# Optimization experiments

Hardware: AMD Instinct MI355X
Metric: run time of the kernel (lower is better)

The kernel has to match this reference:

```python
import jax, jax.numpy as jnp
import numpy as np

B, SEQ, D, N_LAYERS, HEADS, D_FF = 256, 43, 18, 6, 3, 2048
A_MAX, NB = 128, 7
EPS = 1e-6


def _norm(x, a, b):
    mu = x.mean(-1, keepdims=True)
    sd = jnp.std(x, axis=-1, ddof=1, keepdims=True)  # torch std is unbiased
    return a * (x - mu) / (sd + EPS) + b


def _attn(x, Wq, bq, Wk, bk, Wv, bv, Wo, bo, mask):
    b_, s, d = x.shape
    dk = d // HEADS
    def split_heads(W, bb):
        return (x @ W + bb).reshape(b_, s, HEADS, dk).transpose(0, 2, 1, 3)
    q, k, v = split_heads(Wq, bq), split_heads(Wk, bk), split_heads(Wv, bv)
    scores = jnp.einsum('bhqd,bhkd->bhqk', q, k) / jnp.sqrt(jnp.float32(dk))
    scores = jnp.where(mask[:, None, :, :] == 0, -1e9, scores)  # mask [B,1,S] -> [B,1,1,S]
    attn = jax.nn.softmax(scores, axis=-1)
    o = jnp.einsum('bhqk,bhkd->bhqd', attn, v).transpose(0, 2, 1, 3).reshape(b_, s, d)
    return o @ Wo + bo


def setup_inputs() -> dict:
    key = jax.random.key(0)
    ks = iter(jax.random.split(key, 40))
    g = lambda shape, s=0.05: jax.random.normal(next(ks), shape, dtype=jnp.float32) * s
    inp = {
        'src': jax.random.normal(next(ks), (B, SEQ, D), dtype=jnp.float32),
        'mask': jnp.ones((B, 1, SEQ), dtype=jnp.int32),
        'max_atoms': A_MAX,
        'enc_Wq': g((N_LAYERS, D, D)), 'enc_bq': g((N_LAYERS, D)),
        'enc_Wk': g((N_LAYERS, D, D)), 'enc_bk': g((N_LAYERS, D)),
        'enc_Wv': g((N_LAYERS, D, D)), 'enc_bv': g((N_LAYERS, D)),
        'enc_Wo': g((N_LAYERS, D, D)), 'enc_bo': g((N_LAYERS, D)),
        'enc_ln1_a': jnp.ones((N_LAYERS, D), jnp.float32), 'enc_ln1_b': jnp.zeros((N_LAYERS, D), jnp.float32),
        'enc_ln2_a': jnp.ones((N_LAYERS, D), jnp.float32), 'enc_ln2_b': jnp.zeros((N_LAYERS, D), jnp.float32),
        'enc_ffW1': g((N_LAYERS, D, D_FF)), 'enc_ffb1': g((N_LAYERS, D_FF)),
        'enc_ffW2': g((N_LAYERS, D_FF, D)), 'enc_ffb2': g((N_LAYERS, D)),
        'll2_W': g((D, A_MAX)), 'll2_b': g((A_MAX,)),
        'll_W': g((SEQ, A_MAX)), 'll_b': g((A_MAX,)),
        'fl_W': g((2 * A_MAX, NB)), 'fl_b': g((NB,)),
    }
    return inp


def reference(src, enc_Wq, enc_bq, enc_Wk, enc_bk, enc_Wv, enc_bv, enc_Wo, enc_bo,
              enc_ln1_a, enc_ln1_b, enc_ln2_a, enc_ln2_b,
              enc_ffW1, enc_ffb1, enc_ffW2, enc_ffb2,
              ll2_W, ll2_b, ll_W, ll_b, fl_W, fl_b, mask, max_atoms):
    # --- Encoder (dropout=0 at eval; no final norm, as in source) ---
    x = src
    for i in range(N_LAYERS):
        x2 = _norm(x, enc_ln1_a[i], enc_ln1_b[i])
        x = x + _attn(x2, enc_Wq[i], enc_bq[i], enc_Wk[i], enc_bk[i],
                      enc_Wv[i], enc_bv[i], enc_Wo[i], enc_bo[i], mask)
        x2 = _norm(x, enc_ln2_a[i], enc_ln2_b[i])
        x = x + (jax.nn.relu(x2 @ enc_ffW1[i] + enc_ffb1[i]) @ enc_ffW2[i] + enc_ffb2[i])
    # --- EdgeClassify2 ---
    red = x @ ll2_W + ll2_b            # [B, S, A]
    red = red.transpose(0, 2, 1)       # [B, A, S]
    R = red @ ll_W + ll_b              # [B, A, A]; repeat_e[:,i,i,:] == R[:,i,:]
    # final_e[b,i,j] = concat(R[b,i], R[b,j]); fl(concat) = R_i@W1 + R_j@W2 + b (exact)
    W1, W2 = fl_W[:max_atoms], fl_W[max_atoms:]
    P = R @ W1                          # [B, A, nb]
    Q = R @ W2                          # [B, A, nb]
    return P[:, :, None, :] + Q[:, None, :, :] + fl_b  # [B, A, A, nb]
```

## Files before the change

### kernel.cpp

```cpp
#include <hip/hip_runtime.h>
#include <math.h>

namespace {

constexpr int Sq = 43;
constexpr int Dm = 18;
constexpr int Dff = 2048;
constexpr int Am = 128;
constexpr int Nb = 7;
constexpr int NR = 11008;
constexpr int RSZ = NR * Dm;
constexpr float EPSf = 1e-6f;

typedef __attribute__((ext_vector_type(8))) short bf16x8;
typedef __attribute__((ext_vector_type(4))) float f32x4;

__device__ __forceinline__ bf16x8 FRAG(uint4 u) {
    return __builtin_bit_cast(bf16x8, u);
}
__device__ __forceinline__ unsigned BFPK(float a, float b) {
    return (__float_as_uint(a) >> 16) | (__float_as_uint(b) & 0xFFFF0000u);
}

__global__ __launch_bounds__(192) void k_attn(
    int layer,
    const float* __restrict__ Xi, float* __restrict__ Xn,
    float* __restrict__ x2g,
    const int* __restrict__ maskg,
    const float* __restrict__ Wq, const float* __restrict__ bq,
    const float* __restrict__ Wk, const float* __restrict__ bk,
    const float* __restrict__ Wv, const float* __restrict__ bv,
    const float* __restrict__ ln1a, const float* __restrict__ ln1b,
    const float* __restrict__ Wo, const float* __restrict__ bo,
    const float* __restrict__ ln2a, const float* __restrict__ ln2b,
    const float* __restrict__ b2g,
    const float* __restrict__ fW1g, const float* __restrict__ fW2g,
    uint4* __restrict__ W1F, uint4* __restrict__ W2F,
    const float* __restrict__ llW, const float* __restrict__ llb,
    const float* __restrict__ flW, const float* __restrict__ flb,
    const float* __restrict__ ll2b,
    float* __restrict__ Mw, float* __restrict__ PS1, float* __restrict__ QS2)
{
    __shared__ __align__(16) float ks[Sq * 20];
    __shared__ __align__(16) float vs[Sq * 20];
    __shared__ float os[Sq * Dm];
    __shared__ int ms[Sq];
    __shared__ float M[602];
    __shared__ float cc2[14];
    __shared__ float SS[14];

    const int tid = threadIdx.x;
    const int b = blockIdx.x;

    if (b >= 256) {
        if (b < 320) {
            for (int e = (b - 256) * 192 + tid; e < 98304; e += 12288) {
                const int lane = e & 63;
                const int s = (e >> 6) & 1;
                const int t = (e >> 7) & 1;
                const int c = (e >> 8) & 63;
                const int l = e >> 14;
                const int g = lane >> 4, m = lane & 15;
                {
                    const int j = c * 32 + t * 16 + m;
                    unsigned u[4] = {0u, 0u, 0u, 0u};
                    #pragma unroll
                    for (int i = 0; i < 8; i++) {
                        const int k = 8 * g + i;
                        float v = (k < 18)
                            ? fW1g[((size_t)l * Dm + k) * Dff + j] : 0.f;
                        unsigned hb = __float_as_uint(v) & 0xFFFF0000u;
                        unsigned bits;
                        if (s == 0) bits = hb >> 16;
                        else {
                            float lo = v - __uint_as_float(hb);
                            bits = (__float_as_uint(lo) & 0xFFFF0000u) >> 16;
                        }
                        u[i >> 1] |= bits << (16 * (i & 1));
                    }
                    W1F[e] = make_uint4(u[0], u[1], u[2], u[3]);
                }
                {
                    unsigned u[4] = {0u, 0u, 0u, 0u};
                    const int d = (t == 0) ? m : 16 + m;
                    const bool valid = (t == 0) || (m < 2);
                    #pragma unroll
                    for (int i = 0; i < 8; i++) {
                        const int j = c * 32 + 8 * g + i;
                        float v = valid
                            ? fW2g[((size_t)l * Dff + j) * Dm + d] : 0.f;
                        unsigned hb = __float_as_uint(v) & 0xFFFF0000u;
                        unsigned bits;
                        if (s == 0) bits = hb >> 16;
                        else {
                            float lo = v - __uint_as_float(hb);
                            bits = (__float_as_uint(lo) & 0xFFFF0000u) >> 16;
                        }
                        u[i >> 1] |= bits << (16 * (i & 1));
                    }
                    W2F[e] = make_uint4(u[0], u[1], u[2], u[3]);
                }
            }
            return;
        }
        for (int m = tid; m < 602; m += 192) {
            int half = m / 301, rem = m - half * 301;
            int s = rem / 7, n = rem - 7 * s;
            float a = 0.f;
            for (int jj = 0; jj < Am; jj++)
                a += llW[s * Am + jj] * flW[(half * Am + jj) * Nb + n];
            M[m] = a;
        }
        if (tid < 14) {
            int half = tid / 7, n = tid - 7 * (tid / 7);
            float a = 0.f;
            for (int jj = 0; jj < Am; jj++)
                a += llb[jj] * flW[(half * Am + jj) * Nb + n];
            cc2[tid] = a;
        }
        __syncthreads();
        if (tid < 14) {
            int half = tid / 7, n = tid - 7 * (tid / 7);
            float s2 = 0.f;
            for (int s = 0; s < Sq; s++) s2 += M[half * 301 + s * 7 + n];
            SS[tid] = s2;
        }
        __syncthreads();
        for (int m = tid; m < 602; m += 192) Mw[m] = M[m];
        for (int m = tid; m < 896; m += 192) {
            int i = m / 7, n = m - 7 * i;
            PS1[m] = cc2[n] + ll2b[i] * SS[n];
            QS2[m] = cc2[7 + n] + ll2b[i] * SS[7 + n] + flb[n];
        }
        return;
    }

    const float scale = 0.40824829046386296f;
    const int h = tid >> 6;
    const int q = tid & 63;

    if (tid < Sq) ms[tid] = maskg[b * Sq + tid];

    float y[Dm];
    float qv6[6];
    if (q < Sq) {
        const size_t ro = (size_t)(b * Sq + q) * Dm;
        #pragma unroll
        for (int k = 0; k < 9; k++) {
            float2 t = *(const float2*)(Xi + ro + 2 * k);
            y[2 * k] = t.x; y[2 * k + 1] = t.y;
        }
        float mu = 0.f;
        #pragma unroll
        for (int d = 0; d < Dm; d++) mu += y[d];
        mu *= (1.f / Dm);
        float var = 0.f;
        #pragma unroll
        for (int d = 0; d < Dm; d++) { float t = y[d] - mu; var += t * t; }
        var *= (1.f / (Dm - 1));
        float isd = 1.f / (sqrtf(var) + EPSf);
        float x2[Dm];
        #pragma unroll
        for (int d = 0; d < Dm; d++)
            x2[d] = ln1a[layer * Dm + d] * (y[d] - mu) * isd
                  + ln1b[layer * Dm + d];
        const float* wqp = Wq + layer * Dm * Dm;
        const float* wkp = Wk + layer * Dm * Dm;
        const float* wvp = Wv + layer * Dm * Dm;
        #pragma unroll
        for (int dh = 0; dh < 6; dh++) {
            const int d = h * 6 + dh;
            float aq = bq[layer * Dm + d];
            float ak = bk[layer * Dm + d];
            float av = bv[layer * Dm + d];
            #pragma unroll
            for (int dd = 0; dd < Dm; dd++) {
                aq += x2[dd] * wqp[dd * Dm + d];
                ak += x2[dd] * wkp[dd * Dm + d];
                av += x2[dd] * wvp[dd * Dm + d];
            }
            qv6[dh] = aq;
            ks[q * 20 + d] = ak;
            vs[q * 20 + d] = av;
        }
    }
    __syncthreads();

    if (q < Sq) {
        float sum = 0.f;
        float o6[6];
        #pragma unroll
        for (int d = 0; d < 6; d++) o6[d] = 0.f;
        const float q0 = qv6[0], q1 = qv6[1], q2 = qv6[2];
        const float q3 = qv6[3], q4 = qv6[4], q5 = qv6[5];
        for (int j = 0; j < Sq; j++) {
            const float* kr = ks + j * 20 + h * 6;
            const float2 k0 = *(const float2*)(kr);
            const float2 k1 = *(const float2*)(kr + 2);
            const float2 k2 = *(const float2*)(kr + 4);
            float t = q0 * k0.x + q1 * k0.y + q2 * k1.x +
                      q3 * k1.y + q4 * k2.x + q5 * k2.y;
            t *= scale;
            if (ms[j] == 0) t = -1e9f;
            float e = __expf(t);
            sum += e;
            const float* vr = vs + j * 20 + h * 6;
            const float2 v0 = *(const float2*)(vr);
            const float2 v1 = *(const float2*)(vr + 2);
            const float2 v2 = *(const float2*)(vr + 4);
            o6[0] += e * v0.x; o6[1] += e * v0.y; o6[2] += e * v1.x;
            o6[3] += e * v1.y; o6[4] += e * v2.x; o6[5] += e * v2.y;
        }
        float inv = 1.f / sum;
        #pragma unroll
        for (int d = 0; d < 6; d++) os[q * Dm + h * 6 + d] = o6[d] * inv;
    }
    __syncthreads();

    if (h == 0 && q < Sq) {
        const float* wo = Wo + layer * Dm * Dm;
        const float* orow = os + q * Dm;
        float yo[Dm];
        #pragma unroll 3
        for (int d = 0; d < Dm; d++) {
            float t = bo[layer * Dm + d];
            #pragma unroll
            for (int dd = 0; dd < Dm; dd++) t += orow[dd] * wo[dd * Dm + d];
            yo[d] = y[d] + t;
        }
        const size_t ro = (size_t)(b * Sq + q) * Dm;
        #pragma unroll
        for (int d = 0; d < Dm; d++)
            Xn[ro + d] = yo[d] + b2g[layer * Dm + d];
        float mu = 0.f;
        #pragma unroll
        for (int d = 0; d < Dm; d++) mu += yo[d];
        mu *= (1.f / Dm);
        float var = 0.f;
        #pragma unroll
        for (int d = 0; d < Dm; d++) { float t = yo[d] - mu; var += t * t; }
        var *= (1.f / (Dm - 1));
        float isd = 1.f / (sqrtf(var) + EPSf);
        #pragma unroll
        for (int d = 0; d < Dm; d++)
            x2g[ro + d] =
                ln2a[layer * Dm + d] * (yo[d] - mu) * isd + ln2b[layer * Dm + d];
    }
}

__global__ __launch_bounds__(256) void k_ffn(
    int layer, const float* __restrict__ x2g,
    const uint4* __restrict__ W1F, const uint4* __restrict__ W2F,
    const float* __restrict__ fb1g, float* __restrict__ Xn)
{
    __shared__ __align__(16) short Hbuf[4][2][640];

    const int tid  = threadIdx.x;
    const int lane = tid & 63;
    const int wv   = tid >> 6;
    const int g    = lane >> 4;
    const int m    = lane & 15;
    const int row  = blockIdx.x * 16 + m;

    unsigned bh[4] = {0u, 0u, 0u, 0u}, bl[4] = {0u, 0u, 0u, 0u};
    #pragma unroll
    for (int i = 0; i < 8; i++) {
        const int k = 8 * g + i;
        float v = (k < 18) ? x2g[(size_t)row * Dm + k] : 0.f;
        unsigned hbits = __float_as_uint(v) & 0xFFFF0000u;
        float lo = v - __uint_as_float(hbits);
        unsigned lbits = __float_as_uint(lo) & 0xFFFF0000u;
        bh[i >> 1] |= (hbits >> 16) << (16 * (i & 1));
        bl[i >> 1] |= (lbits >> 16) << (16 * (i & 1));
    }
    const bf16x8 Bxhi = FRAG(make_uint4(bh[0], bh[1], bh[2], bh[3]));
    const bf16x8 Bxlo = FRAG(make_uint4(bl[0], bl[1], bl[2], bl[3]));

    f32x4 y0 = {0.f, 0.f, 0.f, 0.f};
    f32x4 y1 = {0.f, 0.f, 0.f, 0.f};
    const uint4* w1b = W1F + (size_t)layer * 16384;
    const uint4* w2b = W2F + (size_t)layer * 16384;
    const float* b1b = fb1g + layer * Dff;
    short* Hh = &Hbuf[wv][0][0];
    short* Hl = &Hbuf[wv][1][0];

    const int c0 = wv * 16;
    for (int c = c0; c < c0 + 16; ++c) {
        #pragma unroll
        for (int t = 0; t < 2; ++t) {
            const uint4 ah = w1b[c * 256 + t * 128 + lane];
            const uint4 al = w1b[c * 256 + t * 128 + 64 + lane];
            f32x4 c1 = {0.f, 0.f, 0.f, 0.f};
            c1 = __builtin_amdgcn_mfma_f32_16x16x32_bf16(FRAG(ah), Bxhi, c1, 0, 0, 0);
            c1 = __builtin_amdgcn_mfma_f32_16x16x32_bf16(FRAG(al), Bxhi, c1, 0, 0, 0);
            c1 = __builtin_amdgcn_mfma_f32_16x16x32_bf16(FRAG(ah), Bxlo, c1, 0, 0, 0);
            const f32x4 bb = *(const f32x4*)(b1b + c * 32 + t * 16 + 4 * g);
            unsigned ph[2], pl[2];
            #pragma unroll
            for (int r2 = 0; r2 < 2; ++r2) {
                float h0 = fmaxf(c1[2 * r2] + bb[2 * r2], 0.f);
                float h1 = fmaxf(c1[2 * r2 + 1] + bb[2 * r2 + 1], 0.f);
                unsigned h0b = __float_as_uint(h0) & 0xFFFF0000u;
                unsigned h1b = __float_as_uint(h1) & 0xFFFF0000u;
                ph[r2] = (h0b >> 16) | h1b;
                float l0 = h0 - __uint_as_float(h0b);
                float l1 = h1 - __uint_as_float(h1b);
                pl[r2] = ((__float_as_uint(l0) & 0xFFFF0000u) >> 16)
                       | (__float_as_uint(l1) & 0xFFFF0000u);
            }
            const int joff = m * 40 + t * 16 + 4 * g;
            *(uint2*)&Hh[joff] = make_uint2(ph[0], ph[1]);
            *(uint2*)&Hl[joff] = make_uint2(pl[0], pl[1]);
        }
        const bf16x8 bH = FRAG(*(const uint4*)&Hh[m * 40 + 8 * g]);
        const bf16x8 bL = FRAG(*(const uint4*)&Hl[m * 40 + 8 * g]);
        const uint4 a0h = w2b[c * 256 + lane];
        const uint4 a0l = w2b[c * 256 + 64 + lane];
        const uint4 a1h = w2b[c * 256 + 128 + lane];
        const uint4 a1l = w2b[c * 256 + 192 + lane];
        y0 = __builtin_amdgcn_mfma_f32_16x16x32_bf16(FRAG(a0h), bH, y0, 0, 0, 0);
        y0 = __builtin_amdgcn_mfma_f32_16x16x32_bf16(FRAG(a0l), bH, y0, 0, 0, 0);
        y0 = __builtin_amdgcn_mfma_f32_16x16x32_bf16(FRAG(a0h), bL, y0, 0, 0, 0);
        y1 = __builtin_amdgcn_mfma_f32_16x16x32_bf16(FRAG(a1h), bH, y1, 0, 0, 0);
        y1 = __builtin_amdgcn_mfma_f32_16x16x32_bf16(FRAG(a1l), bH, y1, 0, 0, 0);
        y1 = __builtin_amdgcn_mfma_f32_16x16x32_bf16(FRAG(a1h), bL, y1, 0, 0, 0);
    }

    #pragma unroll
    for (int r = 0; r < 4; ++r)
        unsafeAtomicAdd(&Xn[(size_t)row * Dm + 4 * g + r], y0[r]);
    if (g == 0) {
        unsafeAtomicAdd(&Xn[(size_t)row * Dm + 16], y1[0]);
        unsafeAtomicAdd(&Xn[(size_t)row * Dm + 17], y1[1]);
    }
}

__global__ __launch_bounds__(256) void k_out(
    const float* __restrict__ xg,
    const float* __restrict__ ll2W,
    const float* __restrict__ Mw, const float* __restrict__ PS1,
    const float* __restrict__ QS2, float* __restrict__ out)
{
    __shared__ float xb[Sq * Dm];
    __shared__ float M[602];
    __shared__ float T[2][Dm][Nb];
    __shared__ float Pc[32 * Nb];
    __shared__ float QBs[Am * Nb];

    const int b = blockIdx.y, chunk = blockIdx.x, tid = threadIdx.x;

    for (int e = tid; e < Sq * Dm; e += 256)
        xb[e] = xg[(size_t)b * (Sq * Dm) + e];
    for (int m = tid; m < 602; m += 256) M[m] = Mw[m];
    __syncthreads();

    for (int m = tid; m < 252; m += 256) {
        int half = m / 126, rem = m - half * 126;
        int d = rem / 7, n = rem - 7 * d;
        float a = 0.f;
        for (int s = 0; s < Sq; s++)
            a += xb[s * Dm + d] * M[half * 301 + s * 7 + n];
        T[half][d][n] = a;
    }
    __syncthreads();

    for (int m = tid; m < 224; m += 256) {
        int il = m / 7, n = m - 7 * il;
        int i = chunk * 32 + il;
        float a = PS1[i * 7 + n];
        #pragma unroll
        for (int d = 0; d < Dm; d++) a += T[0][d][n] * ll2W[d * Am + i];
        Pc[m] = a;
    }
    for (int e = tid; e < 896; e += 256) {
        int jj = e / 7, n = e - 7 * jj;
        float a = QS2[e];
        #pragma unroll
        for (int d = 0; d < Dm; d++) a += T[1][d][n] * ll2W[d * Am + jj];
        QBs[e] = a;
    }
    __syncthreads();

    if (tid < 224) {
        const int e = 4 * tid;
        const float q0 = QBs[e], q1 = QBs[e + 1], q2 = QBs[e + 2], q3 = QBs[e + 3];
        const int n0 = e % 7, n1 = (e + 1) % 7, n2 = (e + 2) % 7, n3 = (e + 3) % 7;
        const size_t base = (size_t)b * (Am * Am * Nb)
                          + (size_t)chunk * 32 * 896 + e;
        for (int il = 0; il < 32; il++) {
            const float* pc = Pc + il * 7;
            float4 v;
            v.x = pc[n0] + q0; v.y = pc[n1] + q1;
            v.z = pc[n2] + q2; v.w = pc[n3] + q3;
            *(float4*)(out + base + (size_t)il * 896) = v;
        }
    }
}

}

extern "C" void kernel_launch(void* const* d_in, const int* in_sizes, int n_in,
                              void* d_out, int out_size, void* d_ws, size_t ws_size,
                              hipStream_t stream)
{
    (void)in_sizes; (void)n_in; (void)out_size; (void)ws_size;

    const float* src  = (const float*)d_in[0];
    const int*   mask = (const int*)  d_in[1];
    const float* Wq   = (const float*)d_in[3];
    const float* bq   = (const float*)d_in[4];
    const float* Wk   = (const float*)d_in[5];
    const float* bk   = (const float*)d_in[6];
    const float* Wv   = (const float*)d_in[7];
    const float* bv   = (const float*)d_in[8];
    const float* Wo   = (const float*)d_in[9];
    const float* bo   = (const float*)d_in[10];
    const float* ln1a = (const float*)d_in[11];
    const float* ln1b = (const float*)d_in[12];
    const float* ln2a = (const float*)d_in[13];
    const float* ln2b = (const float*)d_in[14];
    const float* fW1  = (const float*)d_in[15];
    const float* fb1  = (const float*)d_in[16];
    const float* fW2  = (const float*)d_in[17];
    const float* fb2  = (const float*)d_in[18];
    const float* ll2W = (const float*)d_in[19];
    const float* ll2b = (const float*)d_in[20];
    const float* llW  = (const float*)d_in[21];
    const float* llb  = (const float*)d_in[22];
    const float* flW  = (const float*)d_in[23];
    const float* flb  = (const float*)d_in[24];
    float* out = (float*)d_out;

    float* ws  = (float*)d_ws;
    float* xA  = ws;
    float* xB  = ws + 1 * (size_t)RSZ;
    float* x2g = ws + 2 * (size_t)RSZ;
    uint4* W1F = (uint4*)(ws + 3 * (size_t)RSZ);
    uint4* W2F = W1F + 98304;
    float* Mw  = (float*)(W2F + 98304);
    float* PS1 = Mw + 604;
    float* QS2 = PS1 + 896;

    for (int i = 0; i < 6; i++) {
        const float* Xi = (i == 0) ? src : ((i % 2 == 1) ? xB : xA);
        float*       Xn = (i % 2 == 0) ? xB : xA;
        const int nblk = (i == 0) ? 321 : 256;
        k_attn<<<nblk, 192, 0, stream>>>(i, Xi, Xn, x2g, mask,
                                         Wq, bq, Wk, bk, Wv, bv,
                                         ln1a, ln1b, Wo, bo, ln2a, ln2b, fb2,
                                         fW1, fW2, W1F, W2F,
                                         llW, llb, flW, flb, ll2b,
                                         Mw, PS1, QS2);
        k_ffn<<<688, 256, 0, stream>>>(i, x2g, W1F, W2F, fb1, Xn);
    }
    k_out<<<dim3(4, 256), 256, 0, stream>>>(xA, ll2W, Mw, PS1, QS2, out);
}
```

Measured before the change: 513.3 us.

## Process two row tiles per FFN block and prefetch next weight chunk

The FFN kernel now handles 32 rows per block (two 16-row tiles), so each W1/W2 weight fragment loaded from global memory feeds MFMAs for both tiles, halving weight traffic per row. It also software-prefetches the next chunk's weight fragments into registers while the current chunk computes. The grid is halved to 344 blocks, which reduces parallelism across CUs, and register pressure rises from the doubled accumulators and prefetch buffers.

New measurement: 546.5 us. 6.5% more time.

```diff
diff --git a/kernel.cpp b/kernel.cpp
--- a/kernel.cpp
+++ b/kernel.cpp
@@ -17,9 +17,6 @@
 
 __device__ __forceinline__ bf16x8 FRAG(uint4 u) {
     return __builtin_bit_cast(bf16x8, u);
-}
-__device__ __forceinline__ unsigned BFPK(float a, float b) {
-    return (__float_as_uint(a) >> 16) | (__float_as_uint(b) & 0xFFFF0000u);
 }
 
 __global__ __launch_bounds__(192) void k_attn(
@@ -253,85 +250,114 @@
     const uint4* __restrict__ W1F, const uint4* __restrict__ W2F,
     const float* __restrict__ fb1g, float* __restrict__ Xn)
 {
-    __shared__ __align__(16) short Hbuf[4][2][640];
+    __shared__ __align__(16) short Hbuf[4][2][2][640];
 
     const int tid  = threadIdx.x;
     const int lane = tid & 63;
     const int wv   = tid >> 6;
     const int g    = lane >> 4;
     const int m    = lane & 15;
-    const int row  = blockIdx.x * 16 + m;
-
-    unsigned bh[4] = {0u, 0u, 0u, 0u}, bl[4] = {0u, 0u, 0u, 0u};
+    const int rbase = blockIdx.x * 32;
+
+    bf16x8 Bxhi[2], Bxlo[2];
     #pragma unroll
-    for (int i = 0; i < 8; i++) {
-        const int k = 8 * g + i;
-        float v = (k < 18) ? x2g[(size_t)row * Dm + k] : 0.f;
-        unsigned hbits = __float_as_uint(v) & 0xFFFF0000u;
-        float lo = v - __uint_as_float(hbits);
-        unsigned lbits = __float_as_uint(lo) & 0xFFFF0000u;
-        bh[i >> 1] |= (hbits >> 16) << (16 * (i & 1));
-        bl[i >> 1] |= (lbits >> 16) << (16 * (i & 1));
-    }
-    const bf16x8 Bxhi = FRAG(make_uint4(bh[0], bh[1], bh[2], bh[3]));
-    const bf16x8 Bxlo = FRAG(make_uint4(bl[0], bl[1], bl[2], bl[3]));
-
-    f32x4 y0 = {0.f, 0.f, 0.f, 0.f};
-    f32x4 y1 = {0.f, 0.f, 0.f, 0.f};
+    for (int rt = 0; rt < 2; ++rt) {
+        const int row = rbase + rt * 16 + m;
+        unsigned bh[4] = {0u, 0u, 0u, 0u}, bl[4] = {0u, 0u, 0u, 0u};
+        #pragma unroll
+        for (int i = 0; i < 8; i++) {
+            const int k = 8 * g + i;
+            float v = (k < 18) ? x2g[(size_t)row * Dm + k] : 0.f;
+            unsigned hbits = __float_as_uint(v) & 0xFFFF0000u;
+            float lo = v - __uint_as_float(hbits);
+            unsigned lbits = __float_as_uint(lo) & 0xFFFF0000u;
+            bh[i >> 1] |= (hbits >> 16) << (16 * (i & 1));
+            bl[i >> 1] |= (lbits >> 16) << (16 * (i & 1));
+        }
+        Bxhi[rt] = FRAG(make_uint4(bh[0], bh[1], bh[2], bh[3]));
+        Bxlo[rt] = FRAG(make_uint4(bl[0], bl[1], bl[2], bl[3]));
+    }
+
+    f32x4 y0[2], y1[2];
+    #pragma unroll
+    for (int rt = 0; rt < 2; ++rt) {
+        y0[rt] = (f32x4){0.f, 0.f, 0.f, 0.f};
+        y1[rt] = (f32x4){0.f, 0.f, 0.f, 0.f};
+    }
     const uint4* w1b = W1F + (size_t)layer * 16384;
     const uint4* w2b = W2F + (size_t)layer * 16384;
     const float* b1b = fb1g + layer * Dff;
-    short* Hh = &Hbuf[wv][0][0];
-    short* Hl = &Hbuf[wv][1][0];
 
     const int c0 = wv * 16;
+    uint4 A0 = w1b[c0 * 256 + lane],        A1 = w1b[c0 * 256 + 64 + lane];
+    uint4 A2 = w1b[c0 * 256 + 128 + lane],  A3 = w1b[c0 * 256 + 192 + lane];
+    uint4 C0 = w2b[c0 * 256 + lane],        C1 = w2b[c0 * 256 + 64 + lane];
+    uint4 C2 = w2b[c0 * 256 + 128 + lane],  C3 = w2b[c0 * 256 + 192 + lane];
+
     for (int c = c0; c < c0 + 16; ++c) {
-        #pragma unroll
-        for (int t = 0; t < 2; ++t) {
-            const uint4 ah = w1b[c * 256 + t * 128 + lane];
-            const uint4 al = w1b[c * 256 + t * 128 + 64 + lane];
-            f32x4 c1 = {0.f, 0.f, 0.f, 0.f};
-            c1 = __builtin_amdgcn_mfma_f32_16x16x32_bf16(FRAG(ah), Bxhi, c1, 0, 0, 0);
-            c1 = __builtin_amdgcn_mfma_f32_16x16x32_bf16(FRAG(al), Bxhi, c1, 0, 0, 0);
-            c1 = __builtin_amdgcn_mfma_f32_16x16x32_bf16(FRAG(ah), Bxlo, c1, 0, 0, 0);
-            const f32x4 bb = *(const f32x4*)(b1b + c * 32 + t * 16 + 4 * g);
-            unsigned ph[2], pl[2];
+        const int cn = (c + 1 < c0 + 16) ? c + 1 : c;
+        const uint4 nA0 = w1b[cn * 256 + lane],       nA1 = w1b[cn * 256 + 64 + lane];
+        const uint4 nA2 = w1b[cn * 256 + 128 + lane], nA3 = w1b[cn * 256 + 192 + lane];
+        const uint4 nC0 = w2b[cn * 256 + lane],       nC1 = w2b[cn * 256 + 64 + lane];
+        const uint4 nC2 = w2b[cn * 256 + 128 + lane], nC3 = w2b[cn * 256 + 192 + lane];
+
+        const f32x4 bb0 = *(const f32x4*)(b1b + c * 32 + 4 * g);
+        const f32x4 bb1 = *(const f32x4*)(b1b + c * 32 + 16 + 4 * g);
+
+        #pragma unroll
+        for (int rt = 0; rt < 2; ++rt) {
+            short* Hh = &Hbuf[wv][rt][0][0];
+            short* Hl = &Hbuf[wv][rt][1][0];
             #pragma unroll
-            for (int r2 = 0; r2 < 2; ++r2) {
-                float h0 = fmaxf(c1[2 * r2] + bb[2 * r2], 0.f);
-                float h1 = fmaxf(c1[2 * r2 + 1] + bb[2 * r2 + 1], 0.f);
-                unsigned h0b = __float_as_uint(h0) & 0xFFFF0000u;
-                unsigned h1b = __float_as_uint(h1) & 0xFFFF0000u;
-                ph[r2] = (h0b >> 16) | h1b;
-                float l0 = h0 - __uint_as_float(h0b);
-                float l1 = h1 - __uint_as_float(h1b);
-                pl[r2] = ((__float_as_uint(l0) & 0xFFFF0000u) >> 16)
-                       | (__float_as_uint(l1) & 0xFFFF0000u);
+            for (int t = 0; t < 2; ++t) {
+                const uint4 ah = (t == 0) ? A0 : A2;
+                const uint4 al = (t == 0) ? A1 : A3;
+                const f32x4 bb = (t == 0) ? bb0 : bb1;
+                f32x4 c1 = {0.f, 0.f, 0.f, 0.f};
+                c1 = __builtin_amdgcn_mfma_f32_16x16x32_bf16(FRAG(ah), Bxhi[rt], c1, 0, 0, 0);
+                c1 = __builtin_amdgcn_mfma_f32_16x16x32_bf16(FRAG(al), Bxhi[rt], c1, 0, 0, 0);
+                c1 = __builtin_amdgcn_mfma_f32_16x16x32_bf16(FRAG(ah), Bxlo[rt], c1, 0, 0, 0);
+                unsigned ph[2], pl[2];
+                #pragma unroll
+                for (int r2 = 0; r2 < 2; ++r2) {
+                    float h0 = fmaxf(c1[2 * r2] + bb[2 * r2], 0.f);
+                    float h1 = fmaxf(c1[2 * r2 + 1] + bb[2 * r2 + 1], 0.f);
+                    unsigned h0b = __float_as_uint(h0) & 0xFFFF0000u;
+                    unsigned h1b = __float_as_uint(h1) & 0xFFFF0000u;
+                    ph[r2] = (h0b >> 16) | h1b;
+                    float l0 = h0 - __uint_as_float(h0b);
+                    float l1 = h1 - __uint_as_float(h1b);
+                    pl[r2] = ((__float_as_uint(l0) & 0xFFFF0000u) >> 16)
+                           | (__float_as_uint(l1) & 0xFFFF0000u);
+                }
+                const int joff = m * 40 + t * 16 + 4 * g;
+                *(uint2*)&Hh[joff] = make_uint2(ph[0], ph[1]);
+                *(uint2*)&Hl[joff] = make_uint2(pl[0], pl[1]);
             }
-            const int joff = m * 40 + t * 16 + 4 * g;
-            *(uint2*)&Hh[joff] = make_uint2(ph[0], ph[1]);
-            *(uint2*)&Hl[joff] = make_uint2(pl[0], pl[1]);
-        }
-        const bf16x8 bH = FRAG(*(const uint4*)&Hh[m * 40 + 8 * g]);
-        const bf16x8 bL = FRAG(*(const uint4*)&Hl[m * 40 + 8 * g]);
-        const uint4 a0h = w2b[c * 256 + lane];
-        const uint4 a0l = w2b[c * 256 + 64 + lane];
-        const uint4 a1h = w2b[c * 256 + 128 + lane];
-        const uint4 a1l = w2b[c * 256 + 192 + lane];
-        y0 = __builtin_amdgcn_mfma_f32_16x16x32_bf16(FRAG(a0h), bH, y0, 0, 0, 0);
-        y0 = __builtin_amdgcn_mfma_f32_16x16x32_bf16(FRAG(a0l), bH, y0, 0, 0, 0);
-        y0 = __builtin_amdgcn_mfma_f32_16x16x32_bf16(FRAG(a0h), bL, y0, 0, 0, 0);
-        y1 = __builtin_amdgcn_mfma_f32_16x16x32_bf16(FRAG(a1h), bH, y1, 0, 0, 0);
-        y1 = __builtin_amdgcn_mfma_f32_16x16x32_bf16(FRAG(a1l), bH, y1, 0, 0, 0);
-        y1 = __builtin_amdgcn_mfma_f32_16x16x32_bf16(FRAG(a1h), bL, y1, 0, 0, 0);
+            const bf16x8 bH = FRAG(*(const uint4*)&Hh[m * 40 + 8 * g]);
+            const bf16x8 bL = FRAG(*(const uint4*)&Hl[m * 40 + 8 * g]);
+            y0[rt] = __builtin_amdgcn_mfma_f32_16x16x32_bf16(FRAG(C0), bH, y0[rt], 0, 0, 0);
+            y0[rt] = __builtin_amdgcn_mfma_f32_16x16x32_bf16(FRAG(C1), bH, y0[rt], 0, 0, 0);
+            y0[rt] = __builtin_amdgcn_mfma_f32_16x16x32_bf16(FRAG(C0), bL, y0[rt], 0, 0, 0);
+            y1[rt] = __builtin_amdgcn_mfma_f32_16x16x32_bf16(FRAG(C2), bH, y1[rt], 0, 0, 0);
+            y1[rt] = __builtin_amdgcn_mfma_f32_16x16x32_bf16(FRAG(C3), bH, y1[rt], 0, 0, 0);
+            y1[rt] = __builtin_amdgcn_mfma_f32_16x16x32_bf16(FRAG(C2), bL, y1[rt], 0, 0, 0);
+        }
+
+        A0 = nA0; A1 = nA1; A2 = nA2; A3 = nA3;
+        C0 = nC0; C1 = nC1; C2 = nC2; C3 = nC3;
     }
 
     #pragma unroll
-    for (int r = 0; r < 4; ++r)
-        unsafeAtomicAdd(&Xn[(size_t)row * Dm + 4 * g + r], y0[r]);
-    if (g == 0) {
-        unsafeAtomicAdd(&Xn[(size_t)row * Dm + 16], y1[0]);
-        unsafeAtomicAdd(&Xn[(size_t)row * Dm + 17], y1[1]);
+    for (int rt = 0; rt < 2; ++rt) {
+        const int row = rbase + rt * 16 + m;
+        #pragma unroll
+        for (int r = 0; r < 4; ++r)
+            unsafeAtomicAdd(&Xn[(size_t)row * Dm + 4 * g + r], y0[rt][r]);
+        if (g == 0) {
+            unsafeAtomicAdd(&Xn[(size_t)row * Dm + 16], y1[rt][0]);
+            unsafeAtomicAdd(&Xn[(size_t)row * Dm + 17], y1[rt][1]);
+        }
     }
 }
 
@@ -451,7 +477,7 @@
                                          fW1, fW2, W1F, W2F,
                                          llW, llb, flW, flb, ll2b,
                                          Mw, PS1, QS2);
-        k_ffn<<<688, 256, 0, stream>>>(i, x2g, W1F, W2F, fb1, Xn);
+        k_ffn<<<344, 256, 0, stream>>>(i, x2g, W1F, W2F, fb1, Xn);
     }
     k_out<<<dim3(4, 256), 256, 0, stream>>>(xA, ll2W, Mw, PS1, QS2, out);
 }
```
